# Kernel optimization log

Measured on AMD Instinct MI355X. Metric: run time of the kernel, lower is better.

## Reference

```python
import jax, jax.numpy as jnp
import numpy as np


def _consts():
    # Hypercube vertices: itertools.product([-1,1], repeat=n) order => MSB-first bits.
    def verts(nbits):
        idx = np.arange(2 ** nbits)
        return (((idx[:, None] >> np.arange(nbits - 1, -1, -1)[None, :]) & 1) * 2.0 - 1.0).astype(np.float32)

    hexagrams = verts(6)   # (64, 6)
    q2_verts = verts(2)    # (4, 2)
    q3_verts = verts(3)    # (8, 3)

    # Q2 vertex -> group one-hot, _Q2_TO_GROUP = [2, 1, 1, 0]
    q2_to_group = np.zeros((4, 3), dtype=np.float32)
    for v, g in enumerate([2, 1, 1, 0]):
        q2_to_group[v, g] = 1.0

    # Group anchors: ABSTRACT = mean(hex[63], hex[62]), DYNAMIC = mean(hex[19], hex[21]),
    # CONCRETE = mean(hex[0], hex[8]); then L2-normalized.
    anch = np.stack([
        hexagrams[[63, 62]].mean(0),
        hexagrams[[19, 21]].mean(0),
        hexagrams[[0, 8]].mean(0),
    ]).astype(np.float32)
    anch = anch / np.clip(np.linalg.norm(anch, axis=-1, keepdims=True), 1e-12, None)

    # Walsh-Hadamard popcount masks, pre-divided by their sums -> (64, 3) matrix.
    bits = np.array([bin(i).count('1') for i in range(64)], dtype=np.float32)
    wa = (bits >= 5).astype(np.float32)
    wd = (bits == 3).astype(np.float32)
    wc = (bits <= 1).astype(np.float32)
    wht_mat = np.stack([wa / wa.sum(), wd / wd.sum(), wc / wc.sum()], axis=1)

    return tuple(jnp.asarray(a) for a in (hexagrams, q2_verts, q3_verts, q2_to_group, anch, wht_mat))


def _q3_to_group_init():
    q3_map = np.zeros((8, 3), dtype=np.float32)
    for i in range(8):
        yc = bin(i).count('1')
        if yc == 0:
            q3_map[i, 2] = 1.0
        elif yc == 1:
            q3_map[i, 1] = 1.0
        elif yc == 2:
            q3_map[i, 0] = 0.6
            q3_map[i, 1] = 0.4
        else:
            q3_map[i, 0] = 1.0
    q3_map = q3_map / np.clip(q3_map.sum(axis=1, keepdims=True), 1e-8, None)
    return q3_map


def setup_inputs() -> dict:
    key = jax.random.key(0)
    k_x, k2, k3, k6 = jax.random.split(key, 4)
    B, T, D = 4, 4096, 2048
    s = 1.0 / float(np.sqrt(D))  # torch Linear default init range
    return {
        'x': jax.random.normal(k_x, (B, T, D), dtype=jnp.float32),
        'ln_w': jnp.ones((D,), dtype=jnp.float32),
        'ln_b': jnp.zeros((D,), dtype=jnp.float32),
        'w_q2': jax.random.uniform(k2, (2, D), minval=-s, maxval=s, dtype=jnp.float32),
        'w_q3': jax.random.uniform(k3, (3, D), minval=-s, maxval=s, dtype=jnp.float32),
        'w_q6': jax.random.uniform(k6, (6, D), minval=-s, maxval=s, dtype=jnp.float32),
        'log_temp': jnp.asarray(np.log(0.5), dtype=jnp.float32),
        'log_scale_mix': jnp.zeros((3,), dtype=jnp.float32),
        'q3_to_group': jnp.asarray(_q3_to_group_init()),
        'log_wht_mix': jnp.asarray(-2.0, dtype=jnp.float32),
    }


def _forward(x, ln_w, ln_b, w_q2, w_q3, w_q6, log_temp, log_scale_mix, q3_to_group, log_wht_mix):
    hexa, q2v, q3v, q2g, anch, wht_mat = _consts()

    # LayerNorm (eps = 1e-5, torch default)
    mu = x.mean(-1, keepdims=True)
    var = ((x - mu) ** 2).mean(-1, keepdims=True)
    h = (x - mu) * jax.lax.rsqrt(var + 1e-5) * ln_w + ln_b

    temp = jnp.clip(jnp.exp(log_temp), 0.1, 5.0)

    # Q2 scale: (B,T,2) -> 4 vertices -> 3 groups
    w2 = jax.nn.softmax(jnp.tanh(h @ w_q2.T) @ q2v.T / temp, axis=-1)
    score_q2 = w2 @ q2g

    # Q3 scale: (B,T,3) -> 8 vertices -> learned soft group map
    w3 = jax.nn.softmax(jnp.tanh(h @ w_q3.T) @ q3v.T / temp, axis=-1)
    score_q3 = w3 @ jax.nn.softmax(q3_to_group, axis=-1)

    # Q6 scale: (B,T,6) -> 64 hexagram vertices
    hex_w = jax.nn.softmax(jnp.tanh(h @ w_q6.T) @ hexa.T / temp, axis=-1)
    score_cos = (hex_w @ hexa) @ anch.T            # cosine-sim vs normalized anchors
    score_wht = hex_w @ wht_mat                    # popcount-mask averages
    alpha = jax.nn.sigmoid(log_wht_mix)
    score_q6 = (1.0 - alpha) * score_cos + alpha * score_wht

    mix = jax.nn.softmax(log_scale_mix)
    group_w = jax.nn.softmax(mix[0] * score_q2 + mix[1] * score_q3 + mix[2] * score_q6, axis=-1)

    mg = group_w.mean(axis=(0, 1))
    mh = hex_w.mean(axis=(0, 1))
    lb_loss = jnp.sum(mg * jnp.log(mg + 1e-8)) + 0.1 * jnp.sum(mh * jnp.log(mh + 1e-8))
    return group_w, hex_w, lb_loss


def reference(x, ln_w, ln_b, w_q2, w_q3, w_q6, log_temp, log_scale_mix, q3_to_group, log_wht_mix):
    return _forward(x, ln_w, ln_b, w_q2, w_q3, w_q6, log_temp, log_scale_mix, q3_to_group, log_wht_mix)
```

## Files before the change

kernel.cpp:

```cpp
#include <hip/hip_runtime.h>
#include <math.h>
#include <string.h>

#define D 2048
#define NTOK 16384
#define NROW 11
#define MROWS_U32 (NROW * D / 2)
#define K1_BLOCKS 1024
#define K1_THREADS 256
#define WSTRIDE_U 1036
#define TILE_S 20

#define WS_A 0
#define WS_B 16
#define WS_IT 32
#define WS_ALPHA 33
#define WS_MIX 34
#define WS_M3 40
#define WS_MERGED 64
#define WS_PART (WS_MERGED + MROWS_U32)

typedef __fp16 h2 __attribute__((ext_vector_type(2)));
typedef __fp16 h8 __attribute__((ext_vector_type(8)));
typedef float f32x4 __attribute__((ext_vector_type(4)));

__device__ __forceinline__ float wsum(float v){
#pragma unroll
  for (int m = 1; m < 64; m <<= 1) v += __shfl_xor(v, m, 64);
  return v;
}
__device__ __forceinline__ float wmax(float v){
#pragma unroll
  for (int m = 1; m < 64; m <<= 1) v = fmaxf(v, __shfl_xor(v, m, 64));
  return v;
}
__device__ __forceinline__ float rcp_fast(float x){ return __builtin_amdgcn_rcpf(x); }
__device__ __forceinline__ float tanh_fast(float x){
  float e = __expf(2.0f * x);
  return 1.0f - 2.0f * rcp_fast(e + 1.0f);
}
__device__ __forceinline__ float sload(const float* __restrict__ p){
  return __uint_as_float(__builtin_amdgcn_readfirstlane(__float_as_uint(*p)));
}
__device__ __forceinline__ unsigned int h2u(h2 h){ unsigned int u; memcpy(&u, &h, 4); return u; }

__global__ __launch_bounds__(256) void k0_prep(
    const float* __restrict__ ln_w, const float* __restrict__ ln_b,
    const float* __restrict__ w_q2, const float* __restrict__ w_q3,
    const float* __restrict__ w_q6,
    const float* __restrict__ log_temp, const float* __restrict__ log_scale_mix,
    const float* __restrict__ q3_to_group, const float* __restrict__ log_wht_mix,
    float* __restrict__ ws)
{
  const int tid = threadIdx.x;
  const int k = blockIdx.x;
  unsigned int* wsu = (unsigned int*)ws;
  if (k < NROW){
    const float* row = (k < 2) ? (w_q2 + (size_t)k * D)
                     : (k < 5) ? (w_q3 + (size_t)(k - 2) * D)
                               : (w_q6 + (size_t)(k - 5) * D);
    float pa = 0.f, pb = 0.f;
    for (int i = tid * 2; i < D; i += 512){
      float w0 = row[i], w1 = row[i + 1];
      h2 h = __builtin_amdgcn_cvt_pkrtz(ln_w[i] * w0, ln_w[i + 1] * w1);
      pa += (float)h[0] + (float)h[1];
      pb = fmaf(ln_b[i], w0, pb);
      pb = fmaf(ln_b[i + 1], w1, pb);
      wsu[WS_MERGED + k * 1024 + i / 2] = h2u(h);
    }
    __shared__ float red[8];
    pa = wsum(pa); pb = wsum(pb);
    if ((tid & 63) == 0){ red[tid >> 6] = pa; red[4 + (tid >> 6)] = pb; }
    __syncthreads();
    if (tid == 0){
      ws[WS_A + k] = red[0] + red[1] + red[2] + red[3];
      ws[WS_B + k] = red[4] + red[5] + red[6] + red[7];
    }
  } else if (tid < 64){
    const int lane = tid;
    float q3v = (lane < 24) ? q3_to_group[lane]   : 0.f;
    float sc  = (lane < 3)  ? log_scale_mix[lane] : 0.f;
    float lt  = (lane == 0) ? log_temp[0]         : 0.f;
    float lw  = (lane == 0) ? log_wht_mix[0]      : 0.f;

    if (lane == 0){
      float t = __expf(lt);
      t = fminf(fmaxf(t, 0.1f), 5.0f);
      ws[WS_IT] = 1.0f / t;
      ws[WS_ALPHA] = 1.0f / (1.0f + __expf(-lw));
    }
    float m0 = __shfl(sc, 0, 64), m1 = __shfl(sc, 1, 64), m2 = __shfl(sc, 2, 64);
    if (lane < 3){
      float mm = fmaxf(m0, fmaxf(m1, m2));
      float e0 = __expf(m0 - mm), e1 = __expf(m1 - mm), e2 = __expf(m2 - mm);
      float inv = 1.0f / (e0 + e1 + e2);
      ws[WS_MIX + lane] = ((lane == 0) ? e0 : (lane == 1) ? e1 : e2) * inv;
    }
    if (lane < 24){
      int r = lane / 3, c = lane - r * 3;
      float v0 = __shfl(q3v, r*3 + 0, 64);
      float v1 = __shfl(q3v, r*3 + 1, 64);
      float v2 = __shfl(q3v, r*3 + 2, 64);
      float mx = fmaxf(v0, fmaxf(v1, v2));
      float f0 = __expf(v0 - mx), f1 = __expf(v1 - mx), f2 = __expf(v2 - mx);
      float iv = 1.0f / (f0 + f1 + f2);
      ws[WS_M3 + lane] = ((c == 0) ? f0 : (c == 1) ? f1 : f2) * iv;
    }
  }
}

__global__ __launch_bounds__(256) void k1_main(
    const float* __restrict__ x, const float* __restrict__ ws,
    float* __restrict__ gout, float* __restrict__ hout, float* __restrict__ part)
{
  __shared__ unsigned int sW[NROW * WSTRIDE_U];
  __shared__ float tile[4][16][TILE_S];
  __shared__ float lred[4][68];
  const int tid  = threadIdx.x;
  const int lane = tid & 63;
  const int wid  = tid >> 6;
  const int blk  = blockIdx.x;
  const int tok0 = blk * 16;
  const int n = lane & 15;
  const int q = lane >> 4;

  const float* xp = x + (size_t)(tok0 + n) * D + wid * 512 + q * 8;

  float4 xa[16];
#pragma unroll
  for (int s = 0; s < 8; ++s){
    xa[2*s]     = *(const float4*)(xp + s * 32);
    xa[2*s + 1] = *(const float4*)(xp + s * 32 + 4);
  }

  {
    const uint4* src = (const uint4*)((const unsigned int*)ws + WS_MERGED);
#pragma unroll
    for (int j = 0; j < 11; ++j){
      int idx = tid + j * 256;
      int r = idx >> 8, i = idx & 255;
      *(uint4*)(sW + r * WSTRIDE_U + i * 4) = src[r * 256 + i];
    }
  }

  float sq = 0.f;
  h8 hxA[8], hxB[8];
#pragma unroll
  for (int s = 0; s < 8; ++s){
    float4 f0 = xa[2*s], f1 = xa[2*s + 1];
    sq = fmaf(f0.x,f0.x, fmaf(f0.y,f0.y, fmaf(f0.z,f0.z, fmaf(f0.w,f0.w, sq))));
    sq = fmaf(f1.x,f1.x, fmaf(f1.y,f1.y, fmaf(f1.z,f1.z, fmaf(f1.w,f1.w, sq))));
    h2 p0 = __builtin_amdgcn_cvt_pkrtz(f0.x, f0.y);
    h2 p1 = __builtin_amdgcn_cvt_pkrtz(f0.z, f0.w);
    h2 p2 = __builtin_amdgcn_cvt_pkrtz(f1.x, f1.y);
    h2 p3 = __builtin_amdgcn_cvt_pkrtz(f1.z, f1.w);
    h8 A;
    A[0]=p0[0]; A[1]=p0[1]; A[2]=p1[0]; A[3]=p1[1];
    A[4]=p2[0]; A[5]=p2[1]; A[6]=p3[0]; A[7]=p3[1];
    hxA[s] = A;
  }

  __syncthreads();

#pragma unroll
  for (int s = 0; s < 8; ++s){
    xa[2*s]     = *(const float4*)(xp + (s + 8) * 32);
    xa[2*s + 1] = *(const float4*)(xp + (s + 8) * 32 + 4);
  }

  const int wr = (n < NROW) ? n : (n - NROW);
  const bool is_ones = (n == NROW);
  const uint4 ones4 = make_uint4(0x3C003C00u, 0x3C003C00u, 0x3C003C00u, 0x3C003C00u);
  const unsigned int* wb = sW + wr * WSTRIDE_U + wid * 256 + q * 4;

  f32x4 acc = {0.f, 0.f, 0.f, 0.f};

#pragma unroll
  for (int s = 0; s < 8; ++s){
    uint4 wq = *(const uint4*)(wb + s * 16);
    if (is_ones) wq = ones4;
    h8 B; memcpy(&B, &wq, 16);
    acc = __builtin_amdgcn_mfma_f32_16x16x32_f16(hxA[s], B, acc, 0, 0, 0);
  }

#pragma unroll
  for (int s = 0; s < 8; ++s){
    float4 f0 = xa[2*s], f1 = xa[2*s + 1];
    sq = fmaf(f0.x,f0.x, fmaf(f0.y,f0.y, fmaf(f0.z,f0.z, fmaf(f0.w,f0.w, sq))));
    sq = fmaf(f1.x,f1.x, fmaf(f1.y,f1.y, fmaf(f1.z,f1.z, fmaf(f1.w,f1.w, sq))));
    h2 p0 = __builtin_amdgcn_cvt_pkrtz(f0.x, f0.y);
    h2 p1 = __builtin_amdgcn_cvt_pkrtz(f0.z, f0.w);
    h2 p2 = __builtin_amdgcn_cvt_pkrtz(f1.x, f1.y);
    h2 p3 = __builtin_amdgcn_cvt_pkrtz(f1.z, f1.w);
    h8 A;
    A[0]=p0[0]; A[1]=p0[1]; A[2]=p1[0]; A[3]=p1[1];
    A[4]=p2[0]; A[5]=p2[1]; A[6]=p3[0]; A[7]=p3[1];
    hxB[s] = A;
  }

#pragma unroll
  for (int s = 0; s < 8; ++s){
    uint4 wq = *(const uint4*)(wb + (s + 8) * 16);
    if (is_ones) wq = ones4;
    h8 B; memcpy(&B, &wq, 16);
    acc = __builtin_amdgcn_mfma_f32_16x16x32_f16(hxB[s], B, acc, 0, 0, 0);
  }

  sq += __shfl_xor(sq, 16, 64);
  sq += __shfl_xor(sq, 32, 64);

#pragma unroll
  for (int r = 0; r < 4; ++r) tile[wid][q * 4 + r][n] = acc[r];
  if (lane < 16) tile[wid][lane][16] = sq;

  __syncthreads();

  float a[NROW], bb[NROW];
#pragma unroll
  for (int k = 0; k < NROW; ++k){ a[k] = sload(ws + WS_A + k); bb[k] = sload(ws + WS_B + k); }
  const float it    = sload(ws + WS_IT);
  const float alpha = sload(ws + WS_ALPHA);
  const float mix0 = sload(ws + WS_MIX), mix1 = sload(ws + WS_MIX + 1), mix2 = sload(ws + WS_MIX + 2);
  float M3r[8][3];
#pragma unroll
  for (int r = 0; r < 8; ++r){
#pragma unroll
    for (int g2 = 0; g2 < 3; ++g2) M3r[r][g2] = sload(ws + WS_M3 + r*3 + g2);
  }

  float sgn[6];
#pragma unroll
  for (int j = 0; j < 6; ++j) sgn[j] = ((lane >> (5 - j)) & 1) ? 1.0f : -1.0f;
  const float C5 = 0.44721359549995793f;
  const float A0c[6] = { C5,  C5,  C5,  C5,  C5, 0.f };
  const float A1c[6] = {-0.5f, 0.5f, -0.5f, 0.f, 0.f, 0.5f};
  const float A2c[6] = {-C5, -C5, 0.f, -C5, -C5, -C5};
  float cs0 = 0.f, cs1 = 0.f, cs2 = 0.f;
#pragma unroll
  for (int j = 0; j < 6; ++j){
    cs0 = fmaf(sgn[j], A0c[j], cs0);
    cs1 = fmaf(sgn[j], A1c[j], cs1);
    cs2 = fmaf(sgn[j], A2c[j], cs2);
  }
  const int pc = __popc(lane);
  const float w7c = 1.0f / 7.0f;
  float wh0 = (pc >= 5) ? w7c  : 0.f;
  float wh1 = (pc == 3) ? 0.05f: 0.f;
  float wh2 = (pc <= 1) ? w7c  : 0.f;
  const float m60 = (1.f - alpha)*cs0 + alpha*wh0;
  const float m61 = (1.f - alpha)*cs1 + alpha*wh1;
  const float m62 = (1.f - alpha)*cs2 + alpha*wh2;

  float hsum = 0.f, ga0 = 0.f, ga1 = 0.f, ga2 = 0.f;

#pragma unroll
  for (int i = 0; i < 4; ++i){
    const int tl  = wid * 4 + i;
    const int tok = tok0 + tl;

    float t[12]; float sqv = 0.f;
#pragma unroll
    for (int k = 0; k < 12; ++k) t[k] = 0.f;
#pragma unroll
    for (int hh = 0; hh < 4; ++hh){
      const float* row = &tile[hh][tl][0];
      float4 c0 = *(const float4*)(row);
      float4 c1 = *(const float4*)(row + 4);
      float4 c2 = *(const float4*)(row + 8);
      t[0] += c0.x; t[1] += c0.y; t[2]  += c0.z; t[3]  += c0.w;
      t[4] += c1.x; t[5] += c1.y; t[6]  += c1.z; t[7]  += c1.w;
      t[8] += c2.x; t[9] += c2.y; t[10] += c2.z; t[11] += c2.w;
      sqv += row[16];
    }

    float mean = t[11] * (1.0f / D);
    float var  = fmaf(sqv, 1.0f / D, -mean * mean);
    float rr   = rsqrtf(var + 1e-5f);
    float u[NROW];
#pragma unroll
    for (int k = 0; k < NROW; ++k){
      float d = fmaf(-mean, a[k], t[k]);
      u[k] = tanh_fast(fmaf(rr, d, bb[k]));
    }

    float p01 = u[0] + u[1], m01 = u[0] - u[1];
    float l0 = -p01*it, l1 = -m01*it, l2 = m01*it, l3 = p01*it;
    float mx2 = fmaxf(fmaxf(l0, l1), fmaxf(l2, l3));
    float e0 = __expf(l0-mx2), e1 = __expf(l1-mx2), e2 = __expf(l2-mx2), e3 = __expf(l3-mx2);
    float i2 = rcp_fast(e0 + e1 + e2 + e3);
    float s2g0 = e3 * i2, s2g1 = (e1 + e2) * i2, s2g2 = e0 * i2;

    float l3v[8]; float mx3 = -1e30f;
#pragma unroll
    for (int v = 0; v < 8; ++v){
      float acc3 = ((v & 4) ? u[2] : -u[2]) + ((v & 2) ? u[3] : -u[3]) + ((v & 1) ? u[4] : -u[4]);
      l3v[v] = acc3 * it;
      mx3 = fmaxf(mx3, l3v[v]);
    }
    float w3v[8]; float se3 = 0.f;
#pragma unroll
    for (int v = 0; v < 8; ++v){ w3v[v] = __expf(l3v[v] - mx3); se3 += w3v[v]; }
    float i3 = rcp_fast(se3);
    float s3g0 = 0.f, s3g1 = 0.f, s3g2 = 0.f;
#pragma unroll
    for (int v = 0; v < 8; ++v){
      s3g0 = fmaf(w3v[v], M3r[v][0], s3g0);
      s3g1 = fmaf(w3v[v], M3r[v][1], s3g1);
      s3g2 = fmaf(w3v[v], M3r[v][2], s3g2);
    }
    s3g0 *= i3; s3g1 *= i3; s3g2 *= i3;

    float lg = 0.f;
#pragma unroll
    for (int jj = 0; jj < 6; ++jj) lg = fmaf(sgn[jj], u[5 + jj], lg);
    lg *= it;
    float mx6 = wmax(lg);
    float p   = __expf(lg - mx6);
    float se6 = wsum(p);
    float hw  = p * rcp_fast(se6);
    hout[(size_t)tok * 64 + lane] = hw;
    hsum += hw;
    float s6g0 = wsum(hw * m60);
    float s6g1 = wsum(hw * m61);
    float s6g2 = wsum(hw * m62);

    float g0 = mix0*s2g0 + mix1*s3g0 + mix2*s6g0;
    float g1 = mix0*s2g1 + mix1*s3g1 + mix2*s6g1;
    float g2 = mix0*s2g2 + mix1*s3g2 + mix2*s6g2;
    float gm = fmaxf(g0, fmaxf(g1, g2));
    float y0 = __expf(g0-gm), y1 = __expf(g1-gm), y2 = __expf(g2-gm);
    float gi = rcp_fast(y0 + y1 + y2);
    float gw0 = y0*gi, gw1 = y1*gi, gw2 = y2*gi;
    ga0 += gw0; ga1 += gw1; ga2 += gw2;
    if (lane < 3){
      float val = (lane == 0) ? gw0 : (lane == 1) ? gw1 : gw2;
      gout[(size_t)tok * 3 + lane] = val;
    }
  }

  lred[wid][lane] = hsum;
  if (lane < 3){
    float val = (lane == 0) ? ga0 : (lane == 1) ? ga1 : ga2;
    lred[wid][64 + lane] = val;
  }
  __syncthreads();
  if (tid < 67){
    float v = lred[0][tid] + lred[1][tid] + lred[2][tid] + lred[3][tid];
    part[(size_t)tid * K1_BLOCKS + blk] = v;
  }
}

__global__ __launch_bounds__(1024) void k2_loss(const float* __restrict__ part,
                                                float* __restrict__ lout)
{
  __shared__ float sums[68];
  const int tid = threadIdx.x;
  const int lane = tid & 63;
  const int wid  = tid >> 6;
  for (int jv = wid; jv < 67; jv += 16){
    const float4* p = (const float4*)(part + (size_t)jv * K1_BLOCKS);
    float v = 0.f;
#pragma unroll
    for (int b = 0; b < K1_BLOCKS / 256; ++b){
      float4 q = p[lane + b * 64];
      v += (q.x + q.y) + (q.z + q.w);
    }
    v = wsum(v);
    if (lane == 0) sums[jv] = v;
  }
  __syncthreads();
  if (wid == 0){
    const float inv = 1.0f / (float)NTOK;
    float mh = sums[lane] * inv;
    float term = 0.1f * mh * logf(mh + 1e-8f);
    if (lane < 3){
      float mg = sums[64 + lane] * inv;
      term += mg * logf(mg + 1e-8f);
    }
    float L = wsum(term);
    if (lane == 0) lout[0] = L;
  }
}

extern "C" void kernel_launch(void* const* d_in, const int* in_sizes, int n_in,
                              void* d_out, int out_size, void* d_ws, size_t ws_size,
                              hipStream_t stream)
{
  const float* x             = (const float*)d_in[0];
  const float* ln_w          = (const float*)d_in[1];
  const float* ln_b          = (const float*)d_in[2];
  const float* w_q2          = (const float*)d_in[3];
  const float* w_q3          = (const float*)d_in[4];
  const float* w_q6          = (const float*)d_in[5];
  const float* log_temp      = (const float*)d_in[6];
  const float* log_scale_mix = (const float*)d_in[7];
  const float* q3_to_group   = (const float*)d_in[8];
  const float* log_wht_mix   = (const float*)d_in[9];

  float* out  = (float*)d_out;
  float* gout = out;
  float* hout = out + (size_t)NTOK * 3;
  float* lout = out + (size_t)NTOK * 3 + (size_t)NTOK * 64;
  float* ws   = (float*)d_ws;

  k0_prep<<<12, 256, 0, stream>>>(ln_w, ln_b, w_q2, w_q3, w_q6,
                                  log_temp, log_scale_mix, q3_to_group, log_wht_mix, ws);
  k1_main<<<K1_BLOCKS, K1_THREADS, 0, stream>>>(x, ws, gout, hout, ws + WS_PART);
  k2_loss<<<1, 1024, 0, stream>>>(ws + WS_PART, lout);
}
```

Baseline: 46.36 us.

## Split weight staging into two LDS halves and pipeline x loads in quarters

The shared-memory weight buffer is halved by staging the 11 merged weight rows in two column halves, with a reload and an extra barrier between them. The x register prefetch shrinks from 16 to 8 float4 per thread and is software-pipelined in four chunks interleaved with conversion and MFMA. The aim is lower LDS and VGPR use so more blocks fit per CU, at the cost of an extra sync and a second weight copy per block. Each wave now covers two 256-column spans instead of one contiguous 512-column span.

```diff
diff --git a/kernel.cpp b/kernel.cpp
--- a/kernel.cpp
+++ b/kernel.cpp
@@ -8,7 +8,7 @@
 #define MROWS_U32 (NROW * D / 2)
 #define K1_BLOCKS 1024
 #define K1_THREADS 256
-#define WSTRIDE_U 1036
+#define WSTRIDE2_U 516
 #define TILE_S 20
 
 #define WS_A 0
@@ -109,44 +109,17 @@
   }
 }
 
-__global__ __launch_bounds__(256) void k1_main(
-    const float* __restrict__ x, const float* __restrict__ ws,
-    float* __restrict__ gout, float* __restrict__ hout, float* __restrict__ part)
-{
-  __shared__ unsigned int sW[NROW * WSTRIDE_U];
-  __shared__ float tile[4][16][TILE_S];
-  __shared__ float lred[4][68];
-  const int tid  = threadIdx.x;
-  const int lane = tid & 63;
-  const int wid  = tid >> 6;
-  const int blk  = blockIdx.x;
-  const int tok0 = blk * 16;
-  const int n = lane & 15;
-  const int q = lane >> 4;
-
-  const float* xp = x + (size_t)(tok0 + n) * D + wid * 512 + q * 8;
-
-  float4 xa[16];
-#pragma unroll
-  for (int s = 0; s < 8; ++s){
-    xa[2*s]     = *(const float4*)(xp + s * 32);
-    xa[2*s + 1] = *(const float4*)(xp + s * 32 + 4);
-  }
-
-  {
-    const uint4* src = (const uint4*)((const unsigned int*)ws + WS_MERGED);
-#pragma unroll
-    for (int j = 0; j < 11; ++j){
-      int idx = tid + j * 256;
-      int r = idx >> 8, i = idx & 255;
-      *(uint4*)(sW + r * WSTRIDE_U + i * 4) = src[r * 256 + i];
-    }
-  }
-
-  float sq = 0.f;
-  h8 hxA[8], hxB[8];
-#pragma unroll
-  for (int s = 0; s < 8; ++s){
+__device__ __forceinline__ void load4(const float* __restrict__ xp, int s0, float4* xa){
+#pragma unroll
+  for (int s = 0; s < 4; ++s){
+    xa[2*s]     = *(const float4*)(xp + (s0 + s) * 32);
+    xa[2*s + 1] = *(const float4*)(xp + (s0 + s) * 32 + 4);
+  }
+}
+__device__ __forceinline__ void cvt4(const float4* __restrict__ xa, h8* __restrict__ hx,
+                                     float& sq){
+#pragma unroll
+  for (int s = 0; s < 4; ++s){
     float4 f0 = xa[2*s], f1 = xa[2*s + 1];
     sq = fmaf(f0.x,f0.x, fmaf(f0.y,f0.y, fmaf(f0.z,f0.z, fmaf(f0.w,f0.w, sq))));
     sq = fmaf(f1.x,f1.x, fmaf(f1.y,f1.y, fmaf(f1.z,f1.z, fmaf(f1.w,f1.w, sq))));
@@ -157,50 +130,102 @@
     h8 A;
     A[0]=p0[0]; A[1]=p0[1]; A[2]=p1[0]; A[3]=p1[1];
     A[4]=p2[0]; A[5]=p2[1]; A[6]=p3[0]; A[7]=p3[1];
-    hxA[s] = A;
-  }
-
-  __syncthreads();
-
-#pragma unroll
-  for (int s = 0; s < 8; ++s){
-    xa[2*s]     = *(const float4*)(xp + (s + 8) * 32);
-    xa[2*s + 1] = *(const float4*)(xp + (s + 8) * 32 + 4);
-  }
+    hx[s] = A;
+  }
+}
+
+__global__ __launch_bounds__(256) void k1_main(
+    const float* __restrict__ x, const float* __restrict__ ws,
+    float* __restrict__ gout, float* __restrict__ hout, float* __restrict__ part)
+{
+  __shared__ unsigned int sW[NROW * WSTRIDE2_U];
+  __shared__ float tile[4][16][TILE_S];
+  __shared__ float lred[4][68];
+  const int tid  = threadIdx.x;
+  const int lane = tid & 63;
+  const int wid  = tid >> 6;
+  const int blk  = blockIdx.x;
+  const int tok0 = blk * 16;
+  const int n = lane & 15;
+  const int q = lane >> 4;
+
+  const unsigned int* wsrc = (const unsigned int*)ws + WS_MERGED;
+  const float* xpA = x + (size_t)(tok0 + n) * D + wid * 256 + q * 8;
+  const float* xpB = xpA + 1024;
 
   const int wr = (n < NROW) ? n : (n - NROW);
   const bool is_ones = (n == NROW);
   const uint4 ones4 = make_uint4(0x3C003C00u, 0x3C003C00u, 0x3C003C00u, 0x3C003C00u);
-  const unsigned int* wb = sW + wr * WSTRIDE_U + wid * 256 + q * 4;
-
+  const unsigned int* wb = sW + wr * WSTRIDE2_U + wid * 128 + q * 4;
+
+  float4 xa[8];
+  h8 hxA[4], hxB[4];
+  float sq = 0.f;
   f32x4 acc = {0.f, 0.f, 0.f, 0.f};
 
-#pragma unroll
-  for (int s = 0; s < 8; ++s){
+  load4(xpA, 0, xa);
+
+  {
+    const uint4* src = (const uint4*)wsrc;
+#pragma unroll
+    for (int i = 0; i < 6; ++i){
+      int idx = tid + i * 256;
+      if (idx < 1408){
+        int r = idx >> 7, c = idx & 127;
+        *((uint4*)(sW + r * WSTRIDE2_U) + c) = src[r * 256 + c];
+      }
+    }
+  }
+
+  cvt4(xa, hxA, sq);
+  load4(xpA, 4, xa);
+  __syncthreads();
+
+#pragma unroll
+  for (int s = 0; s < 4; ++s){
     uint4 wq = *(const uint4*)(wb + s * 16);
     if (is_ones) wq = ones4;
     h8 B; memcpy(&B, &wq, 16);
     acc = __builtin_amdgcn_mfma_f32_16x16x32_f16(hxA[s], B, acc, 0, 0, 0);
   }
-
-#pragma unroll
-  for (int s = 0; s < 8; ++s){
-    float4 f0 = xa[2*s], f1 = xa[2*s + 1];
-    sq = fmaf(f0.x,f0.x, fmaf(f0.y,f0.y, fmaf(f0.z,f0.z, fmaf(f0.w,f0.w, sq))));
-    sq = fmaf(f1.x,f1.x, fmaf(f1.y,f1.y, fmaf(f1.z,f1.z, fmaf(f1.w,f1.w, sq))));
-    h2 p0 = __builtin_amdgcn_cvt_pkrtz(f0.x, f0.y);
-    h2 p1 = __builtin_amdgcn_cvt_pkrtz(f0.z, f0.w);
-    h2 p2 = __builtin_amdgcn_cvt_pkrtz(f1.x, f1.y);
-    h2 p3 = __builtin_amdgcn_cvt_pkrtz(f1.z, f1.w);
-    h8 A;
-    A[0]=p0[0]; A[1]=p0[1]; A[2]=p1[0]; A[3]=p1[1];
-    A[4]=p2[0]; A[5]=p2[1]; A[6]=p3[0]; A[7]=p3[1];
-    hxB[s] = A;
-  }
-
-#pragma unroll
-  for (int s = 0; s < 8; ++s){
-    uint4 wq = *(const uint4*)(wb + (s + 8) * 16);
+  cvt4(xa, hxB, sq);
+  load4(xpB, 0, xa);
+#pragma unroll
+  for (int s = 0; s < 4; ++s){
+    uint4 wq = *(const uint4*)(wb + (s + 4) * 16);
+    if (is_ones) wq = ones4;
+    h8 B; memcpy(&B, &wq, 16);
+    acc = __builtin_amdgcn_mfma_f32_16x16x32_f16(hxB[s], B, acc, 0, 0, 0);
+  }
+
+  __syncthreads();
+
+  {
+    const uint4* src = (const uint4*)wsrc;
+#pragma unroll
+    for (int i = 0; i < 6; ++i){
+      int idx = tid + i * 256;
+      if (idx < 1408){
+        int r = idx >> 7, c = idx & 127;
+        *((uint4*)(sW + r * WSTRIDE2_U) + c) = src[r * 256 + 128 + c];
+      }
+    }
+  }
+  cvt4(xa, hxA, sq);
+  load4(xpB, 4, xa);
+  __syncthreads();
+
+#pragma unroll
+  for (int s = 0; s < 4; ++s){
+    uint4 wq = *(const uint4*)(wb + s * 16);
+    if (is_ones) wq = ones4;
+    h8 B; memcpy(&B, &wq, 16);
+    acc = __builtin_amdgcn_mfma_f32_16x16x32_f16(hxA[s], B, acc, 0, 0, 0);
+  }
+  cvt4(xa, hxB, sq);
+#pragma unroll
+  for (int s = 0; s < 4; ++s){
+    uint4 wq = *(const uint4*)(wb + (s + 4) * 16);
     if (is_ones) wq = ones4;
     h8 B; memcpy(&B, &wq, 16);
     acc = __builtin_amdgcn_mfma_f32_16x16x32_f16(hxB[s], B, acc, 0, 0, 0);
```

After: 49.03 us. +5.8%, slower.
